# Kernel optimization log

Measured on AMD Instinct MI355X. Metric: run time of the kernel, lower is better.

Reference implementation:

```python
import jax, jax.numpy as jnp
import numpy as np

SCORE_SCALE = 1.0
Z_LOSS_COEF = 0.001
LB_LOSS_COEF = 0.01
N_EXPERTS = 64
TOP_K = 2
D_MODEL = 4096
T = 8192


def setup_inputs() -> dict:
    key = jax.random.key(0)
    kx, kw = jax.random.split(key)
    x = jax.random.normal(kx, (T, D_MODEL), dtype=jnp.float32)
    W = jax.random.normal(kw, (N_EXPERTS, D_MODEL), dtype=jnp.float32) * (1.0 / np.sqrt(D_MODEL))
    return {"x": x, "W": W}


def reference(x, W):
    # router logits: [T, E]
    logits = jnp.einsum('td,ed->te', x, W) * SCORE_SCALE
    probs = jax.nn.softmax(logits, axis=-1)
    # top-k gating
    topk_scores, topk_experts = jax.lax.top_k(probs, TOP_K)  # [T,k], [T,k]
    denom = jnp.clip(jnp.sum(topk_scores, axis=-1, keepdims=True), 1e-9, None)
    topk_scores = topk_scores / denom
    # z-loss: mean of squared logsumexp
    z_loss = jnp.mean(jax.nn.logsumexp(logits, axis=-1) ** 2)
    # load-balance loss
    importance = jnp.sum(probs, axis=0)  # [E]
    top1 = topk_experts[:, 0]
    load = jax.ops.segment_sum(jnp.ones_like(top1, dtype=jnp.float32), top1,
                               num_segments=N_EXPERTS)  # bincount
    importance = importance / jnp.clip(jnp.sum(importance), 1e-9, None)
    load = load / jnp.clip(jnp.sum(load), 1e-9, None)
    lb_loss = jnp.sum(importance * load) * (N_EXPERTS ** 2)
    router_z_loss = z_loss * Z_LOSS_COEF
    load_balance_loss = lb_loss * LB_LOSS_COEF
    logits_mean = jax.lax.stop_gradient(jnp.mean(logits))
    return (topk_experts, topk_scores, router_z_loss, load_balance_loss, logits_mean)
```

## Files before the change

kernel.cpp:

```cpp
#include <hip/hip_runtime.h>
#include <math.h>


#define NT 8192
#define ND 4096
#define NE 64
#define W_OFF 512
#define WL_OFF (W_OFF + 131072)
#define SLAB2 (W_OFF + 262144)
#define BKD 64
#define SLAB_OFF 512

typedef float f32x4 __attribute__((ext_vector_type(4)));
typedef short s16x8 __attribute__((ext_vector_type(8)));

__device__ __forceinline__ void gload16(const float* g, float* l) {
    __builtin_amdgcn_global_load_lds(
        (const __attribute__((address_space(1))) void*)g,
        (__attribute__((address_space(3))) void*)l, 16, 0, 0);
}

__global__ __launch_bounds__(256)
void convert_w(const float* __restrict__ W, float* __restrict__ ws)
{
    const int s = blockIdx.x * 256 + threadIdx.x;
    const int sg  = s >> 8;
    const int nt  = (s >> 6) & 3;
    const int kb  = (s >> 4) & 3;
    const int e15 = s & 15;
    const int e   = nt * 16 + e15;
    const int k0  = sg * 32 + kb * 8;
    const float* wr = W + (size_t)e * ND + k0;

    union { s16x8 v; ushort u[8]; } h, l;
    #pragma unroll
    for (int j = 0; j < 8; j++) {
        const float v = wr[j];
        const unsigned ub = __float_as_uint(v);
        h.u[j] = (ushort)(ub >> 16);
        const float lo = v - __uint_as_float(ub & 0xffff0000u);
        l.u[j] = (ushort)(__float_as_uint(lo) >> 16);
    }
    *(s16x8*)((ushort*)(ws + W_OFF) + (size_t)s * 8) = h.v;
    *(s16x8*)((ushort*)(ws + WL_OFF) + (size_t)s * 8) = l.v;
}

#define CMFMA(va, vb, bh0, bh1, bl0, bl1)                                    \
    {                                                                        \
        union { s16x8 v; ushort u[8]; } ah, al;                              \
        _Pragma("unroll")                                                    \
        for (int i = 0; i < 4; i++) {                                        \
            const unsigned u0 = __float_as_uint(va[i]);                      \
            ah.u[i] = (ushort)(u0 >> 16);                                    \
            const float l0 = va[i] - __uint_as_float(u0 & 0xffff0000u);      \
            al.u[i] = (ushort)(__float_as_uint(l0) >> 16);                   \
            const unsigned u1 = __float_as_uint(vb[i]);                      \
            ah.u[4 + i] = (ushort)(u1 >> 16);                                \
            const float l1 = vb[i] - __uint_as_float(u1 & 0xffff0000u);      \
            al.u[4 + i] = (ushort)(__float_as_uint(l1) >> 16);               \
        }                                                                    \
        acc0 = __builtin_amdgcn_mfma_f32_16x16x32_bf16(ah.v, bh0, acc0, 0,0,0);\
        acc1 = __builtin_amdgcn_mfma_f32_16x16x32_bf16(ah.v, bh1, acc1, 0,0,0);\
        acc0 = __builtin_amdgcn_mfma_f32_16x16x32_bf16(al.v, bh0, acc0, 0,0,0);\
        acc1 = __builtin_amdgcn_mfma_f32_16x16x32_bf16(al.v, bh1, acc1, 0,0,0);\
        acc0 = __builtin_amdgcn_mfma_f32_16x16x32_bf16(ah.v, bl0, acc0, 0,0,0);\
        acc1 = __builtin_amdgcn_mfma_f32_16x16x32_bf16(ah.v, bl1, acc1, 0,0,0);\
    }

__global__ __launch_bounds__(512, 2)
void pass1_lds(const float* __restrict__ x, float* __restrict__ ws)
{
    __shared__ float  xbuf[2][4096];
    __shared__ ushort wbuf[2][8192];

    const int tid  = threadIdx.x;
    const int wv   = tid >> 6, lane = tid & 63;
    const int mt   = wv >> 1,  ng   = wv & 1;
    const int bq   = blockIdx.x >> 7;
    const int tb   = blockIdx.x & 127;
    const int tok0 = tb * 64;
    const int ntg0 = ng * 2, ntg1 = ng * 2 + 1;
    const int k0   = bq << 10;

    const int t0 = tid >> 4, j0 = tid & 15;
    const int t1 = t0 + 32;
    const float* xg0 = x + (size_t)(tok0 + t0) * ND + k0 + ((j0 ^ (t0 & 7)) << 2);
    const float* xg1 = x + (size_t)(tok0 + t1) * ND + k0 + ((j0 ^ (t1 & 7)) << 2);
    const ushort* whg = (const ushort*)(ws + W_OFF);
    const ushort* wlg = (const ushort*)(ws + WL_OFF);

#define STAGE(bb, cc)                                                        \
    {                                                                        \
        gload16(xg0 + (cc) * 64, &xbuf[bb][tid * 4]);                        \
        gload16(xg1 + (cc) * 64, &xbuf[bb][2048 + tid * 4]);                 \
        const size_t cb = ((size_t)(bq * 32 + (cc) * 2) * 4096)              \
                        + (size_t)tid * 16;                                  \
        gload16((const float*)((const char*)whg + cb),                       \
                (float*)&wbuf[bb][(size_t)tid * 8]);                         \
        gload16((const float*)((const char*)wlg + cb),                       \
                (float*)&wbuf[bb][4096 + (size_t)tid * 8]);                  \
    }

    f32x4 acc0 = {0.f, 0.f, 0.f, 0.f};
    f32x4 acc1 = {0.f, 0.f, 0.f, 0.f};

    const int tl  = mt * 16 + (lane & 15);
    const int swz = lane & 7;
    const int kb4 = (lane >> 4) * 2;

    STAGE(0, 0);
    __syncthreads();

    int b = 0;
    #pragma unroll 1
    for (int c = 0; c < 16; ++c) {
        if (c + 1 < 16) STAGE(b ^ 1, c + 1);
        const char*   xb = (const char*)xbuf[b] + tl * 256;
        const ushort* wb = wbuf[b];
        #pragma unroll
        for (int ks = 0; ks < 2; ++ks) {
            const f32x4 va = *(const f32x4*)(xb + (((ks * 8 + kb4)     ^ swz) << 4));
            const f32x4 vb = *(const f32x4*)(xb + (((ks * 8 + kb4 + 1) ^ swz) << 4));
            const s16x8 bh0 = *(const s16x8*)(wb + ((ks * 4 + ntg0) << 9) + lane * 8);
            const s16x8 bh1 = *(const s16x8*)(wb + ((ks * 4 + ntg1) << 9) + lane * 8);
            const s16x8 bl0 = *(const s16x8*)(wb + 4096 + ((ks * 4 + ntg0) << 9) + lane * 8);
            const s16x8 bl1 = *(const s16x8*)(wb + 4096 + ((ks * 4 + ntg1) << 9) + lane * 8);
            CMFMA(va, vb, bh0, bh1, bl0, bl1);
        }
        __syncthreads();
        b ^= 1;
    }
#undef STAGE

    float* slab = ws + SLAB2 + (size_t)bq * NT * NE;
    const int er = (lane >> 4) * 4;
    #pragma unroll
    for (int r = 0; r < 4; r++) {
        const int token = tok0 + mt * 16 + er + r;
        slab[(size_t)token * NE + ntg0 * 16 + (lane & 15)] = acc0[r];
        slab[(size_t)token * NE + ntg1 * 16 + (lane & 15)] = acc1[r];
    }
}

#define LOADX(dst, off)                                                      \
    {                                                                        \
        _Pragma("unroll")                                                    \
        for (int t = 0; t < 8; t++)                                          \
            dst[t] = *reinterpret_cast<const float4*>(                       \
                xp + (size_t)t * ND + (off));                                \
    }
#define COMP(xv, wptr, wstride)                                              \
    {                                                                        \
        float4 wvv[8];                                                       \
        _Pragma("unroll")                                                    \
        for (int e = 0; e < 8; e++)                                          \
            wvv[e] = *reinterpret_cast<const float4*>((wptr) + e * (wstride));\
        _Pragma("unroll")                                                    \
        for (int e = 0; e < 8; e++) {                                        \
            _Pragma("unroll")                                                \
            for (int t = 0; t < 8; t++) {                                    \
                float a = acc[t][e];                                         \
                a = fmaf(xv[t].x, wvv[e].x, a);                              \
                a = fmaf(xv[t].y, wvv[e].y, a);                              \
                a = fmaf(xv[t].z, wvv[e].z, a);                              \
                a = fmaf(xv[t].w, wvv[e].w, a);                              \
                acc[t][e] = a;                                               \
            }                                                                \
        }                                                                    \
    }

__global__ __launch_bounds__(256, 2)
void pass1_dbuf(const float* __restrict__ x, const float* __restrict__ W,
                float* __restrict__ ws, int kq_bits, int nchunk)
{
    __shared__ float wbuf[2][NE * BKD];
    const int tid  = threadIdx.x;
    const int wave = tid >> 6;
    const int lane = tid & 63;
    const int eg   = lane >> 3;
    const int ks   = lane & 7;
    const int bq   = blockIdx.x >> 8;
    const int tb   = blockIdx.x & 255;
    const int tok0 = tb * 32 + wave * 8;
    const int k0   = bq * (ND >> kq_bits);

    float acc[8][8];
    #pragma unroll
    for (int t = 0; t < 8; t++)
        #pragma unroll
        for (int e = 0; e < 8; e++) acc[t][e] = 0.f;

    const float* xp = x + (size_t)tok0 * ND + k0 + ks * 4;
    #pragma unroll
    for (int r = 0; r < 4; r++) {
        int s = r * 256 + tid;
        gload16(W + (size_t)(s >> 4) * ND + k0 + (s & 15) * 4, &wbuf[0][s << 2]);
    }
    float4 xa[8], xb[8];
    LOADX(xa, 0);
    __syncthreads();

    #pragma unroll 1
    for (int c = 0; c < nchunk; ++c) {
        const int b = c & 1;
        if (c + 1 < nchunk) {
            const int koff = k0 + (c + 1) * BKD;
            #pragma unroll
            for (int r = 0; r < 4; r++) {
                int s = r * 256 + tid;
                gload16(W + (size_t)(s >> 4) * ND + koff + (s & 15) * 4,
                        &wbuf[b ^ 1][s << 2]);
            }
        }
        LOADX(xb, c * BKD + 32);
        COMP(xa, &wbuf[b][(eg * 8) * BKD + ks * 4], BKD);
        if (c + 1 < nchunk) LOADX(xa, (c + 1) * BKD);
        COMP(xb, &wbuf[b][(eg * 8) * BKD + 32 + ks * 4], BKD);
        __syncthreads();
    }

    #pragma unroll
    for (int t = 0; t < 8; t++)
        #pragma unroll
        for (int e = 0; e < 8; e++) {
            float v = acc[t][e];
            v += __shfl_xor(v, 1);
            v += __shfl_xor(v, 2);
            v += __shfl_xor(v, 4);
            acc[t][e] = v;
        }
    float* slab = ws + SLAB_OFF + ((size_t)bq * NT + tok0) * NE;
    #pragma unroll
    for (int t = 0; t < 8; t++) {
        if (ks == t) {
            *reinterpret_cast<float4*>(slab + (size_t)t * NE + eg * 8) =
                make_float4(acc[t][0], acc[t][1], acc[t][2], acc[t][3]);
            *reinterpret_cast<float4*>(slab + (size_t)t * NE + eg * 8 + 4) =
                make_float4(acc[t][4], acc[t][5], acc[t][6], acc[t][7]);
        }
    }
}

__global__ __launch_bounds__(128)
void pass2(float* __restrict__ ws, float* __restrict__ out, int kq, int slab_base)
{
    __shared__ float imp_s[NE];
    __shared__ float load_s[NE];
    const int tid  = threadIdx.x;
    const int lane = tid & 63;
    if (tid < NE) { imp_s[tid] = 0.f; load_s[tid] = 0.f; }
    __syncthreads();

    const int tok = blockIdx.x * 128 + tid;
    float lgv[NE];
    {
        const float* p0 = ws + slab_base + (size_t)tok * NE;
        #pragma unroll
        for (int e4 = 0; e4 < 16; e4++) {
            float4 v = *reinterpret_cast<const float4*>(p0 + e4 * 4);
            lgv[e4*4+0] = v.x; lgv[e4*4+1] = v.y;
            lgv[e4*4+2] = v.z; lgv[e4*4+3] = v.w;
        }
        for (int q = 1; q < kq; q++) {
            const float* pq = ws + slab_base + ((size_t)q * NT + tok) * NE;
            #pragma unroll
            for (int e4 = 0; e4 < 16; e4++) {
                float4 v = *reinterpret_cast<const float4*>(pq + e4 * 4);
                lgv[e4*4+0] += v.x; lgv[e4*4+1] += v.y;
                lgv[e4*4+2] += v.z; lgv[e4*4+3] += v.w;
            }
        }
    }

    float m = -3.0e38f;
    #pragma unroll
    for (int e = 0; e < NE; e++) m = fmaxf(m, lgv[e]);
    float se = 0.f, ssum = 0.f;
    #pragma unroll
    for (int e = 0; e < NE; e++) { ssum += lgv[e]; se += __expf(lgv[e] - m); }
    const float lse = m + __logf(se);
    const float inv = 1.f / se;

    #pragma unroll
    for (int e = 0; e < NE; e++) lgv[e] = __expf(lgv[e] - m) * inv;

    float v1 = -3.0e38f, v2 = -3.0e38f;
    int   i1 = 0, i2 = 0;
    #pragma unroll
    for (int e = 0; e < NE; e++) {
        const float v = lgv[e];
        if (v > v1)      { v2 = v1; i2 = i1; v1 = v; i1 = e; }
        else if (v > v2) { v2 = v;  i2 = e; }
    }
    const float dn = fmaxf(v1 + v2, 1e-9f);

    out[2 * tok]              = (float)i1;
    out[2 * tok + 1]          = (float)i2;
    out[2 * NT + 2 * tok]     = v1 / dn;
    out[2 * NT + 2 * tok + 1] = v2 / dn;
    atomicAdd(&load_s[i1], 1.0f);

    float zv = lse * lse, sv = ssum;
    #pragma unroll
    for (int mk = 1; mk < 64; mk <<= 1) {
        zv += __shfl_xor(zv, mk);
        sv += __shfl_xor(sv, mk);
    }
    if (lane == 0) { atomicAdd(&ws[128], zv); atomicAdd(&ws[129], sv); }

    float impacc = 0.f;
    #pragma unroll
    for (int e = 0; e < NE; e++) {
        float v = lgv[e];
        #pragma unroll
        for (int mk = 1; mk < 64; mk <<= 1) v += __shfl_xor(v, mk);
        if (lane == e) impacc = v;
    }
    atomicAdd(&imp_s[lane], impacc);

    __syncthreads();
    if (tid < NE) {
        atomicAdd(&ws[tid], imp_s[tid]);
        atomicAdd(&ws[NE + tid], load_s[tid]);
    }
}

__global__ void finalize(const float* __restrict__ ws, float* __restrict__ out)
{
    const int l = threadIdx.x;
    const float imp = ws[l];
    const float ld  = ws[NE + l];
    float is = imp, ls = ld;
    #pragma unroll
    for (int mk = 1; mk < 64; mk <<= 1) { is += __shfl_xor(is, mk); ls += __shfl_xor(ls, mk); }
    float v = (imp / fmaxf(is, 1e-9f)) * (ld / fmaxf(ls, 1e-9f));
    #pragma unroll
    for (int mk = 1; mk < 64; mk <<= 1) v += __shfl_xor(v, mk);
    if (l == 0) {
        out[4 * NT]     = (ws[128] / (float)NT) * 0.001f;
        out[4 * NT + 1] = v * (float)(NE * NE) * 0.01f;
        out[4 * NT + 2] = ws[129] / (float)((size_t)NT * NE);
    }
}

extern "C" void kernel_launch(void* const* d_in, const int* in_sizes, int n_in,
                              void* d_out, int out_size, void* d_ws, size_t ws_size,
                              hipStream_t stream) {
    const float* x = (const float*)d_in[0];
    const float* W = (const float*)d_in[1];
    float* out = (float*)d_out;
    float* ws  = (float*)d_ws;

    hipMemsetAsync(ws, 0, 130 * sizeof(float), stream);

    const size_t need4 = (size_t)(SLAB2 + 4ull * NT * NE) * 4;
    if (ws_size >= need4) {
        hipLaunchKernelGGL(convert_w, dim3(128), dim3(256), 0, stream, W, ws);
        hipLaunchKernelGGL(pass1_lds, dim3(4 * 128), dim3(512), 0, stream, x, ws);
        hipLaunchKernelGGL(pass2, dim3(NT / 128), dim3(128), 0, stream,
                           ws, out, 4, SLAB2);
    } else {
        int kq_bits = 2;
        if (ws_size < (SLAB_OFF + 4ull * NT * NE) * 4) kq_bits = 1;
        if (ws_size < (SLAB_OFF + 2ull * NT * NE) * 4) kq_bits = 0;
        const int kq = 1 << kq_bits;
        const int nchunk = (ND >> kq_bits) / BKD;
        hipLaunchKernelGGL(pass1_dbuf, dim3(256 * kq), dim3(256), 0, stream,
                           x, W, ws, kq_bits, nchunk);
        hipLaunchKernelGGL(pass2, dim3(NT / 128), dim3(128), 0, stream,
                           ws, out, kq, SLAB_OFF);
    }
    hipLaunchKernelGGL(finalize, dim3(1), dim3(64), 0, stream, ws, out);
}
```

Before: 56.70 us.

## Restructure pass2 with LDS-transposed logits and fold memset into convert_w

Pass2 now uses one 64-token wave per block. Lanes read the partial-logit slabs with coalesced per-expert loads, reduce them, and transpose the result through padded LDS. Importance is summed through LDS instead of 64 butterfly shuffle reductions, and softmax probabilities for top-k are computed only for the two selected entries. The accumulator memset moves into convert_w on the main path, which removes a separate memset operation. The risks are twice as many blocks, extra LDS traffic, and reliance on convert_w running before pass2 on the same stream.

```diff
diff --git a/kernel.cpp b/kernel.cpp
--- a/kernel.cpp
+++ b/kernel.cpp
@@ -23,6 +23,8 @@
 __global__ __launch_bounds__(256)
 void convert_w(const float* __restrict__ W, float* __restrict__ ws)
 {
+    if (blockIdx.x == 0 && threadIdx.x < 130) ws[threadIdx.x] = 0.f;
+
     const int s = blockIdx.x * 256 + threadIdx.x;
     const int sg  = s >> 8;
     const int nt  = (s >> 6) & 3;
@@ -241,36 +243,28 @@
     }
 }
 
-__global__ __launch_bounds__(128)
+__global__ __launch_bounds__(64)
 void pass2(float* __restrict__ ws, float* __restrict__ out, int kq, int slab_base)
 {
-    __shared__ float imp_s[NE];
+    __shared__ float lgs[64][65];
     __shared__ float load_s[NE];
-    const int tid  = threadIdx.x;
-    const int lane = tid & 63;
-    if (tid < NE) { imp_s[tid] = 0.f; load_s[tid] = 0.f; }
-    __syncthreads();
-
-    const int tok = blockIdx.x * 128 + tid;
+    const int lane = threadIdx.x;
+    const int tok0 = blockIdx.x * 64;
+    load_s[lane] = 0.f;
+
+    #pragma unroll 4
+    for (int t = 0; t < 64; t++) {
+        const size_t off = (size_t)(tok0 + t) * NE + lane;
+        float v = ws[slab_base + off];
+        for (int q = 1; q < kq; q++)
+            v += ws[slab_base + (size_t)q * NT * NE + off];
+        lgs[t][lane] = v;
+    }
+    __syncthreads();
+
     float lgv[NE];
-    {
-        const float* p0 = ws + slab_base + (size_t)tok * NE;
-        #pragma unroll
-        for (int e4 = 0; e4 < 16; e4++) {
-            float4 v = *reinterpret_cast<const float4*>(p0 + e4 * 4);
-            lgv[e4*4+0] = v.x; lgv[e4*4+1] = v.y;
-            lgv[e4*4+2] = v.z; lgv[e4*4+3] = v.w;
-        }
-        for (int q = 1; q < kq; q++) {
-            const float* pq = ws + slab_base + ((size_t)q * NT + tok) * NE;
-            #pragma unroll
-            for (int e4 = 0; e4 < 16; e4++) {
-                float4 v = *reinterpret_cast<const float4*>(pq + e4 * 4);
-                lgv[e4*4+0] += v.x; lgv[e4*4+1] += v.y;
-                lgv[e4*4+2] += v.z; lgv[e4*4+3] += v.w;
-            }
-        }
-    }
+    #pragma unroll
+    for (int e = 0; e < NE; e++) lgv[e] = lgs[lane][e];
 
     float m = -3.0e38f;
     #pragma unroll
@@ -280,9 +274,6 @@
     for (int e = 0; e < NE; e++) { ssum += lgv[e]; se += __expf(lgv[e] - m); }
     const float lse = m + __logf(se);
     const float inv = 1.f / se;
-
-    #pragma unroll
-    for (int e = 0; e < NE; e++) lgv[e] = __expf(lgv[e] - m) * inv;
 
     float v1 = -3.0e38f, v2 = -3.0e38f;
     int   i1 = 0, i2 = 0;
@@ -292,13 +283,24 @@
         if (v > v1)      { v2 = v1; i2 = i1; v1 = v; i1 = e; }
         else if (v > v2) { v2 = v;  i2 = e; }
     }
-    const float dn = fmaxf(v1 + v2, 1e-9f);
-
+    const float p1 = __expf(v1 - m) * inv;
+    const float p2 = __expf(v2 - m) * inv;
+    const float dn = fmaxf(p1 + p2, 1e-9f);
+
+    const int tok = tok0 + lane;
     out[2 * tok]              = (float)i1;
     out[2 * tok + 1]          = (float)i2;
-    out[2 * NT + 2 * tok]     = v1 / dn;
-    out[2 * NT + 2 * tok + 1] = v2 / dn;
+    out[2 * NT + 2 * tok]     = p1 / dn;
+    out[2 * NT + 2 * tok + 1] = p2 / dn;
     atomicAdd(&load_s[i1], 1.0f);
+
+    #pragma unroll
+    for (int e = 0; e < NE; e++) lgs[lane][e] = __expf(lgv[e] - m) * inv;
+    __syncthreads();
+    float ic = 0.f;
+    #pragma unroll
+    for (int t = 0; t < 64; t++) ic += lgs[t][lane];
+    atomicAdd(&ws[lane], ic);
 
     float zv = lse * lse, sv = ssum;
     #pragma unroll
@@ -308,21 +310,8 @@
     }
     if (lane == 0) { atomicAdd(&ws[128], zv); atomicAdd(&ws[129], sv); }
 
-    float impacc = 0.f;
-    #pragma unroll
-    for (int e = 0; e < NE; e++) {
-        float v = lgv[e];
-        #pragma unroll
-        for (int mk = 1; mk < 64; mk <<= 1) v += __shfl_xor(v, mk);
-        if (lane == e) impacc = v;
-    }
-    atomicAdd(&imp_s[lane], impacc);
-
-    __syncthreads();
-    if (tid < NE) {
-        atomicAdd(&ws[tid], imp_s[tid]);
-        atomicAdd(&ws[NE + tid], load_s[tid]);
-    }
+    __syncthreads();
+    atomicAdd(&ws[NE + lane], load_s[lane]);
 }
 
 __global__ void finalize(const float* __restrict__ ws, float* __restrict__ out)
@@ -351,15 +340,14 @@
     float* out = (float*)d_out;
     float* ws  = (float*)d_ws;
 
-    hipMemsetAsync(ws, 0, 130 * sizeof(float), stream);
-
     const size_t need4 = (size_t)(SLAB2 + 4ull * NT * NE) * 4;
     if (ws_size >= need4) {
         hipLaunchKernelGGL(convert_w, dim3(128), dim3(256), 0, stream, W, ws);
         hipLaunchKernelGGL(pass1_lds, dim3(4 * 128), dim3(512), 0, stream, x, ws);
-        hipLaunchKernelGGL(pass2, dim3(NT / 128), dim3(128), 0, stream,
+        hipLaunchKernelGGL(pass2, dim3(NT / 64), dim3(64), 0, stream,
                            ws, out, 4, SLAB2);
     } else {
+        hipMemsetAsync(ws, 0, 130 * sizeof(float), stream);
         int kq_bits = 2;
         if (ws_size < (SLAB_OFF + 4ull * NT * NE) * 4) kq_bits = 1;
         if (ws_size < (SLAB_OFF + 2ull * NT * NE) * 4) kq_bits = 0;
@@ -367,7 +355,7 @@
         const int nchunk = (ND >> kq_bits) / BKD;
         hipLaunchKernelGGL(pass1_dbuf, dim3(256 * kq), dim3(256), 0, stream,
                            x, W, ws, kq_bits, nchunk);
-        hipLaunchKernelGGL(pass2, dim3(NT / 128), dim3(128), 0, stream,
+        hipLaunchKernelGGL(pass2, dim3(NT / 64), dim3(64), 0, stream,
                            ws, out, kq, SLAB_OFF);
     }
     hipLaunchKernelGGL(finalize, dim3(1), dim3(64), 0, stream, ws, out);
```

After: 92.88 us. 1.64x slower.
